# Performance work log

Measured on AMD Instinct MI355X. Metric: run time of the kernel, lower is better.

## Reference

```python
import jax, jax.numpy as jnp
import numpy as np

B, L, C, NH = 512, 196, 384, 12
HW = 14  # window side

def _relative_position_index(h, w):
    coords = np.stack(np.meshgrid(np.arange(h), np.arange(w), indexing='ij'))  # [2,h,w]
    cf = coords.reshape(2, -1)                       # [2, L]
    rel = cf[:, :, None] - cf[:, None, :]            # [2, L, L]
    rel = rel.transpose(1, 2, 0).astype(np.int64)    # [L, L, 2]
    rel[..., 0] += h - 1
    rel[..., 1] += w - 1
    rel[..., 0] *= 2 * w - 1
    return rel.sum(-1)                               # [L, L]

def setup_inputs() -> dict:
    key = jax.random.key(0)
    ks = jax.random.split(key, 5)
    hd = C // NH
    x = jax.random.normal(ks[0], (B, L, C), dtype=jnp.float32)
    # weights stored as [in, out] (equivalent to torch Linear weight.T)
    qkv_w = jax.random.normal(ks[1], (C, 3 * C), dtype=jnp.float32) * (C ** -0.5)
    qkv_b = jnp.zeros((3 * C,), dtype=jnp.float32)
    proj_w = jax.random.normal(ks[2], (C, C), dtype=jnp.float32) * (C ** -0.5)
    proj_b = jnp.zeros((C,), dtype=jnp.float32)
    bias_table = jax.random.normal(ks[3], ((2 * HW - 1) ** 2, NH), dtype=jnp.float32) * 0.02
    rel_index = jnp.asarray(_relative_position_index(HW, HW), dtype=jnp.int32)
    return {"x": x, "qkv_w": qkv_w, "qkv_b": qkv_b, "proj_w": proj_w,
            "proj_b": proj_b, "bias_table": bias_table, "rel_index": rel_index}

def reference(x, qkv_w, qkv_b, proj_w, proj_b, bias_table, rel_index):
    b, l, c = x.shape
    nh = bias_table.shape[1]
    hd = c // nh
    scale = hd ** -0.5
    qkv = (x @ qkv_w + qkv_b).reshape(b, l, 3, nh, hd).transpose(2, 0, 3, 1, 4)  # [3,B,nh,L,hd]
    q, k, v = qkv[0] * scale, qkv[1], qkv[2]
    attn = jnp.einsum('bhqd,bhkd->bhqk', q, k)                 # [B,nh,L,L]
    bias = bias_table[rel_index]                               # [L,L,nh]
    attn = attn + bias.transpose(2, 0, 1)[None]                # add [1,nh,L,L]
    attn = jax.nn.softmax(attn, axis=-1)
    out = jnp.einsum('bhqk,bhkd->bhqd', attn, v)               # [B,nh,L,hd]
    out = out.transpose(0, 2, 1, 3).reshape(b, l, c)
    return out @ proj_w + proj_b
```

## Files before the change

### kernel.cpp

```cpp
#include <hip/hip_runtime.h>
#include <hip/hip_bf16.h>
#include <stdint.h>

typedef __hip_bfloat16 bf16;
typedef __attribute__((ext_vector_type(8))) short frag8;
typedef __attribute__((ext_vector_type(4))) float floatx4;

#define B_WIN 512
#define L_TOK 196
#define C_DIM 384
#define NH    12
#define HD    32
#define QP    208
#define KPAD  224
#define VSTR  236
#define GK    384
#define NST   12
#define QSCALE 0.2550348555f

#if defined(__has_builtin)
#if __has_builtin(__builtin_amdgcn_exp2f)
#define EXP2(x) __builtin_amdgcn_exp2f(x)
#endif
#endif
#ifndef EXP2
#define EXP2(x) exp2f(x)
#endif

__device__ __forceinline__ void async_cp16(const void* g, void* l) {
  __builtin_amdgcn_global_load_lds(
      (const __attribute__((address_space(1))) unsigned int*)g,
      (__attribute__((address_space(3))) unsigned int*)l, 16, 0, 0);
}

__device__ __forceinline__ unsigned short f2bf_bits(float f) {
  bf16 b = __float2bfloat16(f);
  return *(unsigned short*)&b;
}

__device__ __forceinline__ float bfu2f(short u) {
  union { uint32_t i; float f; } c;
  c.i = ((uint32_t)(unsigned short)u) << 16;
  return c.f;
}

__global__ void cast_to_bf16(const float* __restrict__ src, bf16* __restrict__ dst) {
  int i = blockIdx.x * 256 + threadIdx.x;
  float4 v = ((const float4*)src)[i];
  ushort4 o;
  o.x = f2bf_bits(v.x); o.y = f2bf_bits(v.y);
  o.z = f2bf_bits(v.z); o.w = f2bf_bits(v.w);
  ((ushort4*)dst)[i] = o;
}

__global__ void transpose_cast(const float* __restrict__ src, bf16* __restrict__ dst,
                               int K, int N) {
  int idx = blockIdx.x * 256 + threadIdx.x;
  if (idx >= K * N) return;
  int k = idx / N, n = idx - k * N;
  dst[n * K + k] = __float2bfloat16(src[idx]);
}

__global__ void bias_fill(const float* __restrict__ table, const int* __restrict__ rel,
                          bf16* __restrict__ biasb) {
  int idx = blockIdx.x * 256 + threadIdx.x;
  int h = idx / (QP * KPAD);
  int rem = idx - h * (QP * KPAD);
  int q = rem / KPAD, r2 = rem - q * KPAD;
  int kk = r2 >> 5, quad = (r2 >> 3) & 3, i = r2 & 7;
  int k = kk * 32 + quad * 8 + ((i >= 4) ? 4 : 0) + (i & 3);
  float v;
  if (q >= L_TOK)      v = 0.f;
  else if (k >= L_TOK) v = -1e30f;
  else                 v = table[rel[q * L_TOK + k] * NH + h] * 1.4426950408889634f;
  biasb[idx] = __float2bfloat16(v);
}

__device__ __forceinline__ void storev(bf16* p, float v)  { *p = __float2bfloat16(v); }
__device__ __forceinline__ void storev(float* p, float v) { *p = v; }

template <typename OT, int LDA>
__global__ __launch_bounds__(256) void gemm_bt(
    const bf16* __restrict__ A, const bf16* __restrict__ Bt,
    const float* __restrict__ bias, OT* __restrict__ C,
    int M, int N, int qcols, int nbn, int panel) {
  __shared__ __align__(16) bf16 sB[3][128 * 32];
  const int tid = threadIdx.x;
  const int wave = tid >> 6, lane = tid & 63;
  const int SUPER = panel * nbn;
  const int bid = blockIdx.x;
  const int sb = bid / SUPER, rsp = bid - sb * SUPER;
  const long bm = (long)(sb * panel + rsp % panel) * 128;
  const long bn = (long)(rsp / panel) * 128;

  const int colb = lane & 15;
  const int quad = lane >> 4;
  const int srow = wave * 32 + (lane >> 2);
  const int scol = (lane & 3) * 8;
  const bf16* gB = Bt + (bn + srow) * (long)GK + scol;

  const int wr = (wave & 1) * 64;
  const int wc = (wave >> 1) * 64;
  const bf16* gAf = A + (bm + wr + colb) * (long)LDA + quad * 8;

  floatx4 acc[4][4];
#pragma unroll
  for (int i = 0; i < 4; i++)
#pragma unroll
    for (int j = 0; j < 4; j++) acc[i][j] = (floatx4)(0.f);

#define STAGEB(s, buf)                                                       \
  do {                                                                       \
    _Pragma("unroll")                                                        \
    for (int j = 0; j < 2; j++)                                              \
      async_cp16(gB + (size_t)j * 16 * GK + (s) * 32,                        \
                 &sB[buf][(wave * 32 + j * 16) * 32]);                       \
  } while (0)
#define LOADA(dst, s)                                                        \
  do {                                                                       \
    _Pragma("unroll")                                                        \
    for (int mi = 0; mi < 4; mi++)                                           \
      dst[mi] = *(const frag8*)(gAf + (size_t)mi * 16 * LDA + (s) * 32);     \
  } while (0)

  frag8 af[4], afn[4];
  STAGEB(0, 0);
  asm volatile("" ::: "memory");
  LOADA(af, 0);
  asm volatile("" ::: "memory");
  STAGEB(1, 1);
  asm volatile("s_waitcnt vmcnt(2)" ::: "memory");
  __builtin_amdgcn_s_barrier();

  int cur = 0;
#pragma unroll
  for (int t = 0; t < NST; ++t) {
    const int sa = (t + 1 < NST) ? t + 1 : NST - 1;
    LOADA(afn, sa);
    const int sb2 = (t + 2 < NST) ? t + 2 : NST - 1;
    int nb = cur + 2; if (nb >= 3) nb -= 3;
    STAGEB(sb2, nb);

    frag8 bfr[4];
#pragma unroll
    for (int ni = 0; ni < 4; ni++)
      bfr[ni] = *(const frag8*)&sB[cur][(wc + ni * 16 + colb) * 32 + quad * 8];
#pragma unroll
    for (int mi = 0; mi < 4; mi++)
#pragma unroll
      for (int ni = 0; ni < 4; ni++)
        acc[mi][ni] = __builtin_amdgcn_mfma_f32_16x16x32_bf16(af[mi], bfr[ni], acc[mi][ni], 0, 0, 0);
#pragma unroll
    for (int mi = 0; mi < 4; mi++) af[mi] = afn[mi];

    if (t + 1 < NST) {
      asm volatile("s_waitcnt vmcnt(6)" ::: "memory");
      __builtin_amdgcn_s_barrier();
    }
    cur = (cur == 2) ? 0 : cur + 1;
  }
#undef STAGEB
#undef LOADA

#pragma unroll
  for (int ni = 0; ni < 4; ni++) {
    const long col = bn + wc + ni * 16 + colb;
    const float bv = bias[col];
#pragma unroll
    for (int mi = 0; mi < 4; mi++)
#pragma unroll
      for (int r = 0; r < 4; r++) {
        const long row = bm + wr + mi * 16 + quad * 4 + r;
        float val = acc[mi][ni][r] + bv;
        if (col < qcols) val *= QSCALE;
        storev(&C[row * N + col], val);
      }
  }
}

__global__ __launch_bounds__(256) void attn_win(
    bf16* __restrict__ qkv, const bf16* __restrict__ biasb) {
  __shared__ __align__(16) bf16 kL[KPAD * 32];
  __shared__ __align__(16) bf16 vT[HD * VSTR];
  const int b = blockIdx.x, h = blockIdx.y;
  const int tid = threadIdx.x, wave = tid >> 6, lane = tid & 63;
  bf16* base = qkv + (size_t)b * L_TOK * (3 * C_DIM);

  const int colb = lane & 15;
  const int quad = lane >> 4;
  const int rsub = quad * 4;
  const int kswz = (quad ^ ((colb >> 1) & 3)) * 8;

  const bf16* vbase = base + 2 * C_DIM + h * HD;
  const int r0a = tid >> 2, c8a = (tid & 3) * 8;
  const bf16* ga = vbase + (size_t)(2 * r0a) * (3 * C_DIM) + c8a;
  uint4 a0 = *(const uint4*)ga;
  uint4 a1 = *(const uint4*)(ga + 3 * C_DIM);
  const int i1 = tid + 256;
  const bool h1 = i1 < 392;
  const int r0b = h1 ? (i1 >> 2) : r0a, c8b = h1 ? (i1 & 3) * 8 : c8a;
  const bf16* gb = vbase + (size_t)(2 * r0b) * (3 * C_DIM) + c8b;
  uint4 b0 = make_uint4(0, 0, 0, 0), b1 = make_uint4(0, 0, 0, 0);
  if (h1) { b0 = *(const uint4*)gb; b1 = *(const uint4*)(gb + 3 * C_DIM); }

  for (int c = wave; c < 14; c += 4) {
    const int j = c * 16 + (lane >> 2);
    const int slot = lane & 3;
    const int t = j >> 4, qd = (j >> 2) & 3, rr = j & 3;
    int k = (t >> 1) * 32 + qd * 8 + (t & 1) * 4 + rr;
    if (k > L_TOK - 1) k = L_TOK - 1;
    const int sj = (j >> 1) & 3;
    const bf16* src = base + (size_t)k * (3 * C_DIM) + C_DIM + h * HD + ((slot ^ sj) * 8);
    async_cp16(src, &kL[c * 512]);
  }

  {
    ushort ea0[8], ea1[8];
    *(uint4*)ea0 = a0; *(uint4*)ea1 = a1;
#pragma unroll
    for (int e = 0; e < 8; e++) {
      uint32_t pack = (uint32_t)ea0[e] | ((uint32_t)ea1[e] << 16);
      *(uint32_t*)&vT[(c8a + e) * VSTR + 2 * r0a] = pack;
    }
    if (h1) {
      ushort eb0[8], eb1[8];
      *(uint4*)eb0 = b0; *(uint4*)eb1 = b1;
#pragma unroll
      for (int e = 0; e < 8; e++) {
        uint32_t pack = (uint32_t)eb0[e] | ((uint32_t)eb1[e] << 16);
        *(uint32_t*)&vT[(c8b + e) * VSTR + 2 * r0b] = pack;
      }
    }
  }
  for (int idx = tid; idx < HD * 14; idx += 256) {
    int d = idx / 14, pr = idx - d * 14;
    *(uint32_t*)&vT[d * VSTR + L_TOK + 2 * pr] = 0;
  }
  __syncthreads();

  const bf16* biasB = biasb + (size_t)h * QP * KPAD;

#pragma unroll
  for (int ii = 0; ii < 4; ii++) {
    const int rg = wave + 4 * ii;
    if (rg < 13) {
      const int row0 = rg * 16;
      int qrow = row0 + colb; if (qrow > L_TOK - 1) qrow = L_TOK - 1;
      const frag8 aq = *(const frag8*)(base + (size_t)qrow * (3 * C_DIM) + h * HD + quad * 8);
      const bf16* bRow = biasB + (size_t)(row0 + colb) * KPAD;

      floatx4 o0 = (floatx4)(0.f), o1 = (floatx4)(0.f);
      float lsum = 0.f;
#pragma unroll
      for (int kk = 0; kk < 7; kk++) {
        const frag8 k0 = *(const frag8*)&kL[((2 * kk) * 16 + colb) * 32 + kswz];
        const frag8 k1 = *(const frag8*)&kL[((2 * kk + 1) * 16 + colb) * 32 + kswz];
        floatx4 s0 = __builtin_amdgcn_mfma_f32_16x16x32_bf16(k0, aq, (floatx4)(0.f), 0, 0, 0);
        floatx4 s1 = __builtin_amdgcn_mfma_f32_16x16x32_bf16(k1, aq, (floatx4)(0.f), 0, 0, 0);
        const frag8 bb = *(const frag8*)&bRow[kk * 32 + quad * 8];
        frag8 ap;
#pragma unroll
        for (int e = 0; e < 4; e++) {
          float p = EXP2(s0[e] + bfu2f(bb[e]));
          lsum += p;
          ap[e] = (short)f2bf_bits(p);
        }
#pragma unroll
        for (int e = 0; e < 4; e++) {
          float p = EXP2(s1[e] + bfu2f(bb[4 + e]));
          lsum += p;
          ap[4 + e] = (short)f2bf_bits(p);
        }
        const frag8 bv0 = *(const frag8*)&vT[colb * VSTR + kk * 32 + quad * 8];
        const frag8 bv1 = *(const frag8*)&vT[(16 + colb) * VSTR + kk * 32 + quad * 8];
        o0 = __builtin_amdgcn_mfma_f32_16x16x32_bf16(ap, bv0, o0, 0, 0, 0);
        o1 = __builtin_amdgcn_mfma_f32_16x16x32_bf16(ap, bv1, o1, 0, 0, 0);
      }
      lsum += __shfl_xor(lsum, 16, 64);
      lsum += __shfl_xor(lsum, 32, 64);
      const float rl = 1.0f / lsum;
#pragma unroll
      for (int r = 0; r < 4; r++) {
        const float rn = __shfl(rl, rsub + r, 64);
        const int grow = row0 + rsub + r;
        if (grow < L_TOK) {
          base[(size_t)grow * (3 * C_DIM) + h * HD + colb] = __float2bfloat16(o0[r] * rn);
          base[(size_t)grow * (3 * C_DIM) + h * HD + 16 + colb] = __float2bfloat16(o1[r] * rn);
        }
      }
    }
  }
}

extern "C" void kernel_launch(void* const* d_in, const int* in_sizes, int n_in,
                              void* d_out, int out_size, void* d_ws, size_t ws_size,
                              hipStream_t stream) {
  const float* x      = (const float*)d_in[0];
  const float* qkv_w  = (const float*)d_in[1];
  const float* qkv_b  = (const float*)d_in[2];
  const float* proj_w = (const float*)d_in[3];
  const float* proj_b = (const float*)d_in[4];
  const float* btab   = (const float*)d_in[5];
  const int*   relidx = (const int*)d_in[6];
  float* out = (float*)d_out;

  const size_t M = (size_t)B_WIN * L_TOK;
  char* ws = (char*)d_ws;
  size_t off = 0;
  bf16*  qkv   = (bf16*)(ws + off);  off += M * 1152 * 2;
  bf16*  wT1   = (bf16*)(ws + off);  off += (size_t)1152 * 384 * 2;
  bf16*  wT2   = (bf16*)(ws + off);  off += (size_t)384 * 384 * 2;
  bf16*  biasb = (bf16*)(ws + off);  off += (size_t)NH * QP * KPAD * 2;

  bf16* xb = (ws_size >= off + M * C_DIM * sizeof(bf16))
                 ? (bf16*)(ws + off) : (bf16*)d_out;

  cast_to_bf16<<<(int)(M * C_DIM / 4 / 256), 256, 0, stream>>>(x, xb);
  transpose_cast<<<(384 * 1152 + 255) / 256, 256, 0, stream>>>(qkv_w, wT1, 384, 1152);
  transpose_cast<<<(384 * 384 + 255) / 256, 256, 0, stream>>>(proj_w, wT2, 384, 384);
  bias_fill<<<(NH * QP * KPAD) / 256, 256, 0, stream>>>(btab, relidx, biasb);

  gemm_bt<bf16, 384><<<784 * 9, 256, 0, stream>>>(xb, wT1, qkv_b, qkv,
                                                  (int)M, 1152, C_DIM, 9, 28);
  attn_win<<<dim3(B_WIN, NH), 256, 0, stream>>>(qkv, biasb);
  gemm_bt<float, 1152><<<784 * 3, 256, 0, stream>>>(qkv, wT2, proj_b, out,
                                                    (int)M, 384, 0, 3, 28);
}
```

Baseline: 676.6 us.

## Enlarge GEMM tile to 256x128 and stage A through LDS with async copies

```diff
diff --git a/kernel.cpp b/kernel.cpp
--- a/kernel.cpp
+++ b/kernel.cpp
@@ -84,74 +84,66 @@
     const bf16* __restrict__ A, const bf16* __restrict__ Bt,
     const float* __restrict__ bias, OT* __restrict__ C,
     int M, int N, int qcols, int nbn, int panel) {
+  __shared__ __align__(16) bf16 sA[3][256 * 32];
   __shared__ __align__(16) bf16 sB[3][128 * 32];
   const int tid = threadIdx.x;
   const int wave = tid >> 6, lane = tid & 63;
   const int SUPER = panel * nbn;
   const int bid = blockIdx.x;
   const int sb = bid / SUPER, rsp = bid - sb * SUPER;
-  const long bm = (long)(sb * panel + rsp % panel) * 128;
+  const long bm = (long)(sb * panel + rsp % panel) * 256;
   const long bn = (long)(rsp / panel) * 128;
 
   const int colb = lane & 15;
   const int quad = lane >> 4;
-  const int srow = wave * 32 + (lane >> 2);
-  const int scol = (lane & 3) * 8;
-  const bf16* gB = Bt + (bn + srow) * (long)GK + scol;
-
-  const int wr = (wave & 1) * 64;
-  const int wc = (wave >> 1) * 64;
-  const bf16* gAf = A + (bm + wr + colb) * (long)LDA + quad * 8;
-
-  floatx4 acc[4][4];
+  const int srw = lane >> 2;
+  const int scl = (lane & 3) * 8;
+  const bf16* gA = A + (bm + wave * 64 + srw) * (long)LDA + scl;
+  const bf16* gB = Bt + (bn + wave * 32 + srw) * (long)GK + scl;
+
+  const int wr = wave * 64;
+
+  floatx4 acc[4][8];
 #pragma unroll
   for (int i = 0; i < 4; i++)
 #pragma unroll
-    for (int j = 0; j < 4; j++) acc[i][j] = (floatx4)(0.f);
-
-#define STAGEB(s, buf)                                                       \
+    for (int j = 0; j < 8; j++) acc[i][j] = (floatx4)(0.f);
+
+#define STAGE(s, buf)                                                        \
   do {                                                                       \
+    _Pragma("unroll")                                                        \
+    for (int jj = 0; jj < 4; jj++)                                           \
+      async_cp16(gA + (size_t)jj * 16 * LDA + (s) * 32,                      \
+                 &sA[buf][(wave * 64 + jj * 16) * 32]);                      \
     _Pragma("unroll")                                                        \
     for (int j = 0; j < 2; j++)                                              \
       async_cp16(gB + (size_t)j * 16 * GK + (s) * 32,                        \
                  &sB[buf][(wave * 32 + j * 16) * 32]);                       \
   } while (0)
-#define LOADA(dst, s)                                                        \
-  do {                                                                       \
-    _Pragma("unroll")                                                        \
-    for (int mi = 0; mi < 4; mi++)                                           \
-      dst[mi] = *(const frag8*)(gAf + (size_t)mi * 16 * LDA + (s) * 32);     \
-  } while (0)
-
-  frag8 af[4], afn[4];
-  STAGEB(0, 0);
-  asm volatile("" ::: "memory");
-  LOADA(af, 0);
-  asm volatile("" ::: "memory");
-  STAGEB(1, 1);
-  asm volatile("s_waitcnt vmcnt(2)" ::: "memory");
+
+  STAGE(0, 0);
+  STAGE(1, 1);
+  asm volatile("s_waitcnt vmcnt(6)" ::: "memory");
   __builtin_amdgcn_s_barrier();
 
   int cur = 0;
 #pragma unroll
   for (int t = 0; t < NST; ++t) {
-    const int sa = (t + 1 < NST) ? t + 1 : NST - 1;
-    LOADA(afn, sa);
-    const int sb2 = (t + 2 < NST) ? t + 2 : NST - 1;
+    const int s2 = (t + 2 < NST) ? t + 2 : NST - 1;
     int nb = cur + 2; if (nb >= 3) nb -= 3;
-    STAGEB(sb2, nb);
-
-    frag8 bfr[4];
-#pragma unroll
-    for (int ni = 0; ni < 4; ni++)
-      bfr[ni] = *(const frag8*)&sB[cur][(wc + ni * 16 + colb) * 32 + quad * 8];
+    STAGE(s2, nb);
+
+    frag8 af[4];
 #pragma unroll
     for (int mi = 0; mi < 4; mi++)
-#pragma unroll
-      for (int ni = 0; ni < 4; ni++)
-        acc[mi][ni] = __builtin_amdgcn_mfma_f32_16x16x32_bf16(af[mi], bfr[ni], acc[mi][ni], 0, 0, 0);
-#pragma unroll
-    for (int mi = 0; mi < 4; mi++) af[mi] = afn[mi];
+      af[mi] = *(const frag8*)&sA[cur][(wr + mi * 16 + colb) * 32 + quad * 8];
+#pragma unroll
+    for (int ni = 0; ni < 8; ni++) {
+      const frag8 bfr = *(const frag8*)&sB[cur][(ni * 16 + colb) * 32 + quad * 8];
+#pragma unroll
+      for (int mi = 0; mi < 4; mi++)
+        acc[mi][ni] = __builtin_amdgcn_mfma_f32_16x16x32_bf16(af[mi], bfr, acc[mi][ni], 0, 0, 0);
+    }
 
     if (t + 1 < NST) {
       asm volatile("s_waitcnt vmcnt(6)" ::: "memory");
@@ -159,12 +151,11 @@
     }
     cur = (cur == 2) ? 0 : cur + 1;
   }
-#undef STAGEB
-#undef LOADA
-
-#pragma unroll
-  for (int ni = 0; ni < 4; ni++) {
-    const long col = bn + wc + ni * 16 + colb;
+#undef STAGE
+
+#pragma unroll
+  for (int ni = 0; ni < 8; ni++) {
+    const long col = bn + ni * 16 + colb;
     const float bv = bias[col];
 #pragma unroll
     for (int mi = 0; mi < 4; mi++)
@@ -320,9 +311,9 @@
   transpose_cast<<<(384 * 384 + 255) / 256, 256, 0, stream>>>(proj_w, wT2, 384, 384);
   bias_fill<<<(NH * QP * KPAD) / 256, 256, 0, stream>>>(btab, relidx, biasb);
 
-  gemm_bt<bf16, 384><<<784 * 9, 256, 0, stream>>>(xb, wT1, qkv_b, qkv,
-                                                  (int)M, 1152, C_DIM, 9, 28);
+  gemm_bt<bf16, 384><<<392 * 9, 256, 0, stream>>>(xb, wT1, qkv_b, qkv,
+                                                  (int)M, 1152, C_DIM, 9, 14);
   attn_win<<<dim3(B_WIN, NH), 256, 0, stream>>>(qkv, biasb);
-  gemm_bt<float, 1152><<<784 * 3, 256, 0, stream>>>(qkv, wT2, proj_b, out,
-                                                    (int)M, 384, 0, 3, 28);
-}
+  gemm_bt<float, 1152><<<392 * 3, 256, 0, stream>>>(qkv, wT2, proj_b, out,
+                                                    (int)M, 384, 0, 3, 14);
+}
```

After: 629.0 us. 1.08x faster.
